# Kernel tuning notes

Measured on AMD Instinct MI355X. Metric: run time of the kernel, lower is better.

Reference implementation:

```python
import jax, jax.numpy as jnp
from jax import lax
import numpy as np

CONF_THRES = 0.55
IOU_THRES = 0.45
MAX_DET = 1000
MAX_WH = 7680.0   # class offset for class-aware NMS (agnostic=False)
K = 4096          # NMS candidate cap (yolov5 max_nms analogue, jit-static)
IMG = 640         # letterboxed network input size
B, N, NC = 16, 25200, 80


def setup_inputs() -> dict:
    key = jax.random.key(0)
    k1, k2, k3, k4 = jax.random.split(key, 4)
    cxcy = jax.random.uniform(k1, (B, N, 2), jnp.float32, 0.0, IMG)
    wh = jax.random.uniform(k2, (B, N, 2), jnp.float32, 2.0, 120.0)
    obj = jax.random.uniform(k3, (B, N, 1), jnp.float32) ** 4
    cls = jax.random.uniform(k4, (B, N, NC), jnp.float32)
    pred = jnp.concatenate([cxcy, wh, obj, cls], axis=-1)  # [B, N, 5+NC]
    return {"pred": pred, "img0_h": 1080, "img0_w": 1920}


def xywh2xyxy(x):
    cx, cy, w, h = x[..., 0], x[..., 1], x[..., 2], x[..., 3]
    return jnp.stack([cx - w / 2, cy - h / 2, cx + w / 2, cy + h / 2], axis=-1)


def box_iou(a, b):
    # a: [K,4], b: [K,4] xyxy -> [K,K]
    lt = jnp.maximum(a[:, None, :2], b[None, :, :2])
    rb = jnp.minimum(a[:, None, 2:], b[None, :, 2:])
    wh = jnp.clip(rb - lt, 0.0)
    inter = wh[..., 0] * wh[..., 1]
    area_a = (a[:, 2] - a[:, 0]) * (a[:, 3] - a[:, 1])
    area_b = (b[:, 2] - b[:, 0]) * (b[:, 3] - b[:, 1])
    return inter / (area_a[:, None] + area_b[None, :] - inter + 1e-7)


def _nms_image(p, img0_h, img0_w):
    # p: [N, 5+NC]
    obj = p[:, 4]
    cls_conf = p[:, 5:] * obj[:, None]          # conf = obj * cls
    conf = cls_conf.max(axis=-1)
    cls_id = cls_conf.argmax(axis=-1)
    valid = (obj > CONF_THRES) & (conf > CONF_THRES)
    score = jnp.where(valid, conf, -1.0)
    # top-K candidates, sorted by confidence (descending)
    top_scores, top_idx = lax.top_k(score, K)
    boxes = xywh2xyxy(p[top_idx, :4])           # [K,4]
    cl = cls_id[top_idx].astype(p.dtype)        # [K]
    iou = box_iou(boxes + cl[:, None] * MAX_WH, boxes + cl[:, None] * MAX_WH)
    idx = jnp.arange(K)
    keep0 = top_scores > 0.0

    def body(i, keep):
        # suppress i if a higher-scoring kept box overlaps it too much
        sup = jnp.any(keep & (idx < i) & (iou[:, i] > IOU_THRES))
        return keep.at[i].set(keep[i] & ~sup)

    keep = lax.fori_loop(0, K, body, keep0)
    kept_score = jnp.where(keep, top_scores, -1.0)
    fs, fi = lax.top_k(kept_score, MAX_DET)
    fb = boxes[fi]                              # [MAX_DET,4]
    fc = cl[fi]
    fvalid = fs > 0.0
    # scale_boxes: letterboxed 640x640 -> original img0
    gain = min(IMG / img0_h, IMG / img0_w)
    pad_x = (IMG - img0_w * gain) / 2
    pad_y = (IMG - img0_h * gain) / 2
    fb = (fb - jnp.array([pad_x, pad_y, pad_x, pad_y], fb.dtype)) / gain
    fb = jnp.clip(fb, 0.0, jnp.array([img0_w, img0_h, img0_w, img0_h], fb.dtype))
    fb = jnp.round(fb)
    det = jnp.concatenate([fb, fs[:, None], fc[:, None]], axis=-1)  # [MAX_DET,6]
    return jnp.where(fvalid[:, None], det, 0.0)


def reference(pred, img0_h, img0_w):
    return jax.vmap(lambda p: _nms_image(p, img0_h, img0_w))(pred)
```

## Files before the change

### kernel.cpp

```cpp
#include <hip/hip_runtime.h>

#define BB 16
#define NN 25200
#define NC 80
#define ROWL 85
#define KTOP 4096
#define MAXDET 1000
#define CONF_T 0.55f
#define IOU_T 0.45f
#define MAX_WH_F 7680.0f
#define CNT_STRIDE 32
#define PCNT_STRIDE 16
#define CCAP 256
#define NBIN 2048

#define OFF_CNT   81920
#define OFF_KCNT  83968
#define OFF_BUCK  86016
#define OFF_KEPT  2707456
#define ZERO_WORDS 21504

__global__ void zero_kernel(unsigned int* __restrict__ w) {
  w[blockIdx.x * 256 + threadIdx.x] = 0u;
}

__global__ __launch_bounds__(256) void score_kernel(const float* __restrict__ pred,
                             unsigned long long* __restrict__ buckets,
                             unsigned int* __restrict__ pcnt,
                             unsigned int* __restrict__ cnt) {
  const int b = blockIdx.y;
  const int lane = threadIdx.x & 63;
  const int a0 = blockIdx.x * 256 + (threadIdx.x & ~63);
  const int a = a0 + lane;
  const int g = lane >> 3;
  const int gl = lane & 7;
  const float* __restrict__ pb = pred + (size_t)b * NN * ROWL;
  float obj = 0.0f;
  if (a < NN) obj = pb[(size_t)a * ROWL + 4];
  unsigned long long mask = __ballot(obj > CONF_T);
  unsigned int nvacc = 0;
  while (mask) {
    unsigned long long sv = 0ull;
    #pragma unroll
    for (int q = 0; q < 8; ++q) {
      int sq = 255;
      if (mask) { sq = __ffsll(mask) - 1; mask &= mask - 1; }
      sv |= (unsigned long long)(unsigned)sq << (8 * q);
    }
    const int s0v = (int)(sv & 0xFF);
    const int sgv = (int)((sv >> (8 * g)) & 0xFF);
    const bool act = (sgv != 255);
    const int srow = act ? sgv : s0v;
    const int aa = a0 + srow;
    const float objg = __shfl(obj, srow, 64);
    const float* __restrict__ row = pb + (size_t)aa * ROWL;
    float best = -1.0f; int bi = gl;
    #pragma unroll
    for (int u = 0; u < 10; ++u) {
      float v = row[5 + gl + 8 * u] * objg;
      if (v > best) { best = v; bi = gl + 8 * u; }
    }
    #pragma unroll
    for (int off = 1; off <= 4; off <<= 1) {
      float ov = __shfl_xor(best, off, 64);
      int oi = __shfl_xor(bi, off, 64);
      if (ov > best || (ov == best && oi < bi)) { best = ov; bi = oi; }
    }
    bool emit = act && (gl == 0) && (best > CONF_T);
    if (emit) {
      unsigned long long key =
          ((unsigned long long)__float_as_uint(best) << 32) |
          ((unsigned long long)((~(unsigned)aa) & 0xFFFFu) << 16) |
          (unsigned long long)(unsigned)bi;
      unsigned int slot = atomicAdd(&pcnt[(b * NC + bi) * PCNT_STRIDE], 1u);
      if (slot < CCAP)
        buckets[((size_t)(b * NC + bi) << 8) + slot] = key;
    }
    unsigned long long em = __ballot(emit);
    if (lane == 0) nvacc += (unsigned int)__popcll(em);
  }
  if (lane == 0 && nvacc)
    atomicAdd(&cnt[b * CNT_STRIDE], nvacc);
}

__device__ __forceinline__ bool iou_sup(float ax1, float ay1, float ax2, float ay2,
                                        float aar, float bx1, float by1, float bx2,
                                        float by2, float bar) {
  float ltx = fmaxf(ax1, bx1), lty = fmaxf(ay1, by1);
  float rbx = fminf(ax2, bx2), rby = fminf(ay2, by2);
  float wv = rbx - ltx; wv = wv > 0.0f ? wv : 0.0f;
  float hv = rby - lty; hv = hv > 0.0f ? hv : 0.0f;
  float inter = wv * hv;
  float iou = inter / (aar + bar - inter + 1e-7f);
  return iou > IOU_T;
}

__global__ __launch_bounds__(64) void class_nms_kernel(
    const float* __restrict__ pred,
    const unsigned long long* __restrict__ buckets,
    const unsigned int* __restrict__ pcnt,
    const unsigned int* __restrict__ cnt,
    unsigned long long* __restrict__ kept,
    unsigned int* __restrict__ kcnt) {
  const int c = blockIdx.x;
  const int b = blockIdx.y;
  const int lane = threadIdx.x;
  const unsigned long long* __restrict__ bk = buckets + ((size_t)(b * NC + c) << 8);
  unsigned long long v0 = bk[lane];
  unsigned int pc = pcnt[(b * NC + c) * PCNT_STRIDE];
  const int count = (int)cnt[b * CNT_STRIDE];
  int n_c = (int)(pc < (unsigned)CCAP ? pc : (unsigned)CCAP);
  const float* __restrict__ pb = pred + (size_t)b * NN * ROWL;
  const float offc = (float)c * MAX_WH_F;

  if (n_c == 0) return;

  if (n_c <= 64 && count <= KTOP) {
    if (lane >= n_c) v0 = 0ull;
    for (int k2 = 2; k2 <= 64; k2 <<= 1) {
      for (int j = k2 >> 1; j >= 1; j >>= 1) {
        unsigned long long vo = __shfl_xor(v0, j, 64);
        bool desc = ((lane & k2) == 0);
        bool low = ((lane & j) == 0);
        if ((desc == low) ? (vo > v0) : (vo < v0)) v0 = vo;
      }
    }
    float x1 = 0.f, y1 = 0.f, x2 = 0.f, y2 = 0.f, aar = 0.f;
    const bool inr = (lane < n_c);
    if (inr) {
      unsigned int lo = (unsigned int)v0;
      int aa = (int)((~(lo >> 16)) & 0xFFFFu);
      const float* row = pb + (size_t)aa * ROWL;
      float cx = row[0], cy = row[1], w2 = row[2], h2 = row[3];
      x1 = (cx - w2 / 2.0f) + offc;
      y1 = (cy - h2 / 2.0f) + offc;
      x2 = (cx + w2 / 2.0f) + offc;
      y2 = (cy + h2 / 2.0f) + offc;
      aar = (x2 - x1) * (y2 - y1);
    }
    unsigned long long rowreg = 0ull;
    for (int i2 = 0; i2 < n_c; ++i2) {
      float bx1 = __shfl(x1, i2, 64), by1 = __shfl(y1, i2, 64);
      float bx2 = __shfl(x2, i2, 64), by2 = __shfl(y2, i2, 64);
      float bar = __shfl(aar, i2, 64);
      bool sup = inr && (lane > i2) &&
                 iou_sup(bx1, by1, bx2, by2, bar, x1, y1, x2, y2, aar);
      unsigned long long rm = __ballot(sup);
      if (lane == i2) rowreg = rm;
    }
    unsigned long long cand = (n_c >= 64) ? ~0ull : ((1ull << n_c) - 1ull);
    unsigned long long keepm = 0ull;
    while (cand) {
      int i = __ffsll(cand) - 1;
      keepm |= (1ull << i);
      unsigned long long rowi = __shfl(rowreg, i, 64);
      cand &= ~rowi;
      cand &= ~(1ull << i);
    }
    int keep0 = (int)((keepm >> lane) & 1ull);
    unsigned long long m0 = __ballot(keep0 != 0);
    int tot = (int)__popcll(m0);
    unsigned int base3 = 0;
    if (lane == 0) base3 = atomicAdd(&kcnt[b * CNT_STRIDE], (unsigned int)tot);
    base3 = (unsigned int)__shfl((int)base3, 0, 64);
    if (keep0) {
      unsigned int slot = base3 + (unsigned int)__popcll(m0 & ((1ull << lane) - 1ull));
      if (slot < (unsigned)KTOP) kept[(size_t)b * KTOP + slot] = v0;
    }
    return;
  }

  unsigned long long v[4];
  #pragma unroll
  for (int r = 0; r < 4; ++r) {
    int e = (r << 6) + lane;
    v[r] = (e < n_c) ? bk[e] : 0ull;
  }
  if (count > KTOP) {
    unsigned long long T = 0ull;
    for (int bit = 63; bit >= 0; --bit) {
      unsigned long long T2 = T | (1ull << bit);
      int cge = 0;
      for (int c2 = 0; c2 < NC; ++c2) {
        unsigned int p2 = pcnt[(b * NC + c2) * PCNT_STRIDE];
        int n2 = (int)(p2 < (unsigned)CCAP ? p2 : (unsigned)CCAP);
        const unsigned long long* bk2 = buckets + ((size_t)(b * NC + c2) << 8);
        for (int base2 = 0; base2 < n2; base2 += 64) {
          int i = base2 + lane;
          bool ge = (i < n2) && (bk2[i] >= T2);
          cge += (int)__popcll(__ballot(ge));
        }
      }
      if (cge >= KTOP) T = T2;
    }
    #pragma unroll
    for (int r = 0; r < 4; ++r) if (v[r] < T) v[r] = 0ull;
    n_c = 0;
    #pragma unroll
    for (int r = 0; r < 4; ++r) n_c += (int)__popcll(__ballot(v[r] != 0ull));
    if (n_c == 0) return;
  }
  for (int k2 = 2; k2 <= 256; k2 <<= 1) {
    if (k2 == 256) {
      #pragma unroll
      for (int r = 0; r < 2; ++r) {
        unsigned e = (unsigned)((r << 6) + lane);
        bool desc = ((e & k2) == 0);
        unsigned long long lo_ = v[r], hi_ = v[r + 2];
        bool sw = desc ? (lo_ < hi_) : (lo_ > hi_);
        v[r] = sw ? hi_ : lo_; v[r + 2] = sw ? lo_ : hi_;
      }
    }
    if (k2 >= 128) {
      #pragma unroll
      for (int rr = 0; rr < 2; ++rr) {
        int r = rr * 2;
        unsigned e = (unsigned)((r << 6) + lane);
        bool desc = ((e & k2) == 0);
        unsigned long long lo_ = v[r], hi_ = v[r + 1];
        bool sw = desc ? (lo_ < hi_) : (lo_ > hi_);
        v[r] = sw ? hi_ : lo_; v[r + 1] = sw ? lo_ : hi_;
      }
    }
    int j0 = (k2 >> 1) < 32 ? (k2 >> 1) : 32;
    for (int j = j0; j >= 1; j >>= 1) {
      #pragma unroll
      for (int r = 0; r < 4; ++r) {
        unsigned e = (unsigned)((r << 6) + lane);
        unsigned long long vo = __shfl_xor(v[r], j, 64);
        bool desc = ((e & k2) == 0);
        bool low = ((e & j) == 0);
        if ((desc == low) ? (vo > v[r]) : (vo < v[r])) v[r] = vo;
      }
    }
  }
  float x1r[4], y1r[4], x2r[4], y2r[4], ar[4];
  int keepr[4];
  #pragma unroll
  for (int r = 0; r < 4; ++r) {
    int e = (r << 6) + lane;
    keepr[r] = 0; x1r[r] = 0.f; y1r[r] = 0.f; x2r[r] = 0.f; y2r[r] = 0.f; ar[r] = 0.f;
    if (e < n_c) {
      unsigned int lo = (unsigned int)v[r];
      int aa = (int)((~(lo >> 16)) & 0xFFFFu);
      const float* row = pb + (size_t)aa * ROWL;
      float cx = row[0], cy = row[1], w2 = row[2], h2 = row[3];
      x1r[r] = (cx - w2 / 2.0f) + offc;
      y1r[r] = (cy - h2 / 2.0f) + offc;
      x2r[r] = (cx + w2 / 2.0f) + offc;
      y2r[r] = (cy + h2 / 2.0f) + offc;
      ar[r] = (x2r[r] - x1r[r]) * (y2r[r] - y1r[r]);
      keepr[r] = 1;
    }
  }
  for (int i2 = 0; i2 < n_c; ++i2) {
    int ci = i2 >> 6, li = i2 & 63;
    int ki; float bx1v, by1v, bx2v, by2v, bav;
    #define BCAST(R) { ki = __shfl(keepr[R], li, 64); bx1v = __shfl(x1r[R], li, 64); \
                       by1v = __shfl(y1r[R], li, 64); bx2v = __shfl(x2r[R], li, 64); \
                       by2v = __shfl(y2r[R], li, 64); bav = __shfl(ar[R], li, 64); }
    switch (ci) {
      case 0: BCAST(0); break;
      case 1: BCAST(1); break;
      case 2: BCAST(2); break;
      default: BCAST(3); break;
    }
    #undef BCAST
    if (!ki) continue;
    #pragma unroll
    for (int r = 0; r < 4; ++r) {
      int e = (r << 6) + lane;
      if (keepr[r] && e > i2 &&
          iou_sup(bx1v, by1v, bx2v, by2v, bav, x1r[r], y1r[r], x2r[r], y2r[r], ar[r]))
        keepr[r] = 0;
    }
  }
  unsigned long long m[4];
  int tot = 0;
  #pragma unroll
  for (int r = 0; r < 4; ++r) {
    m[r] = __ballot(keepr[r] != 0);
    tot += (int)__popcll(m[r]);
  }
  unsigned int base3 = 0;
  if (lane == 0) base3 = atomicAdd(&kcnt[b * CNT_STRIDE], (unsigned int)tot);
  base3 = (unsigned int)__shfl((int)base3, 0, 64);
  unsigned int start = base3;
  #pragma unroll
  for (int r = 0; r < 4; ++r) {
    if (keepr[r]) {
      unsigned int slot = start + (unsigned int)__popcll(m[r] & ((1ull << lane) - 1ull));
      if (slot < (unsigned)KTOP) kept[(size_t)b * KTOP + slot] = v[r];
    }
    start += (unsigned int)__popcll(m[r]);
  }
}

__global__ __launch_bounds__(1024) void finalize_kernel(
    const float* __restrict__ pred,
    const unsigned long long* __restrict__ kept,
    const unsigned int* __restrict__ kcnt,
    const int* __restrict__ ihp, const int* __restrict__ iwp,
    float* __restrict__ out) {
  __shared__ unsigned int hist[NBIN];
  __shared__ unsigned int sufx[NBIN];
  __shared__ unsigned int curs[NBIN];
  __shared__ unsigned int wsum[16], woff[16];
  __shared__ unsigned long long skey[KTOP];
  const int b = blockIdx.x;
  const int tid = threadIdx.x;
  const int lane = tid & 63;
  const int w = tid >> 6;
  unsigned int kcr = kcnt[b * CNT_STRIDE];
  const int kc = (int)(kcr < (unsigned)KTOP ? kcr : (unsigned)KTOP);
  const unsigned long long* __restrict__ kb = kept + (size_t)b * KTOP;

  hist[2 * tid] = 0u; hist[2 * tid + 1] = 0u;
  __syncthreads();

  unsigned long long myk[4];
  int myb[4];
  #pragma unroll
  for (int r = 0; r < 4; ++r) {
    int i = tid + (r << 10);
    myb[r] = -1; myk[r] = 0ull;
    if (i < kc) {
      unsigned long long k = kb[i];
      int bin = (int)((k >> 44) & (unsigned long long)(NBIN - 1));
      myk[r] = k; myb[r] = bin;
      atomicAdd(&hist[bin], 1u);
    }
  }
  __syncthreads();

  unsigned int h0 = hist[2 * tid], h1 = hist[2 * tid + 1];
  unsigned int v = h0 + h1;
  #pragma unroll
  for (int off = 1; off < 64; off <<= 1) {
    unsigned int o = __shfl_down(v, off, 64);
    if (lane + off < 64) v += o;
  }
  if (lane == 0) wsum[w] = v;
  __syncthreads();
  if (tid < 16) {
    unsigned int s = 0;
    for (int j = tid + 1; j < 16; ++j) s += wsum[j];
    woff[tid] = s;
  }
  __syncthreads();
  unsigned int incl = v + woff[w];
  unsigned int excl = incl - (h0 + h1);
  sufx[2 * tid] = excl + h1;
  sufx[2 * tid + 1] = excl;
  curs[2 * tid] = excl + h1;
  curs[2 * tid + 1] = excl;
  __syncthreads();

  #pragma unroll
  for (int r = 0; r < 4; ++r) {
    if (myb[r] >= 0) {
      unsigned int p = atomicAdd(&curs[myb[r]], 1u);
      skey[p] = myk[r];
    }
  }
  __syncthreads();

  const int h = ihp[0], w3 = iwp[0];
  const double gd = fmin(640.0 / (double)h, 640.0 / (double)w3);
  const float gain = (float)gd;
  const float padx = (float)((640.0 - (double)w3 * gd) * 0.5);
  const float pady = (float)((640.0 - (double)h * gd) * 0.5);
  const float wf = (float)w3, hf = (float)h;
  #pragma unroll
  for (int r = 0; r < 4; ++r) {
    if (myb[r] >= 0) {
      unsigned long long k = myk[r];
      unsigned int gstart = sufx[myb[r]];
      unsigned int gcnt = hist[myb[r]];
      unsigned int rank = gstart;
      for (unsigned int j = 0; j < gcnt; ++j)
        rank += (skey[gstart + j] > k) ? 1u : 0u;
      if (rank < MAXDET) {
        unsigned int lo = (unsigned int)k;
        int aa = (int)((~(lo >> 16)) & 0xFFFFu);
        int cls = (int)(lo & 0xFFFFu);
        float score = __uint_as_float((unsigned int)(k >> 32));
        const float* row = pred + ((size_t)b * NN + aa) * ROWL;
        float cx = row[0], cy = row[1], wd = row[2], ht = row[3];
        float x1 = cx - wd / 2.0f, y1 = cy - ht / 2.0f;
        float x2 = cx + wd / 2.0f, y2 = cy + ht / 2.0f;
        x1 = rintf(fminf(fmaxf((x1 - padx) / gain, 0.0f), wf));
        y1 = rintf(fminf(fmaxf((y1 - pady) / gain, 0.0f), hf));
        x2 = rintf(fminf(fmaxf((x2 - padx) / gain, 0.0f), wf));
        y2 = rintf(fminf(fmaxf((y2 - pady) / gain, 0.0f), hf));
        float* o = out + ((size_t)b * MAXDET + (int)rank) * 6;
        o[0] = x1; o[1] = y1; o[2] = x2; o[3] = y2;
        o[4] = score; o[5] = (float)cls;
      }
    }
  }
  for (int i = kc + tid; i < MAXDET; i += 1024) {
    float* o = out + ((size_t)b * MAXDET + i) * 6;
    o[0] = 0.0f; o[1] = 0.0f; o[2] = 0.0f; o[3] = 0.0f; o[4] = 0.0f; o[5] = 0.0f;
  }
}

extern "C" void kernel_launch(void* const* d_in, const int* in_sizes, int n_in,
                              void* d_out, int out_size, void* d_ws, size_t ws_size,
                              hipStream_t stream) {
  const float* pred = (const float*)d_in[0];
  const int* ih = (const int*)d_in[1];
  const int* iw = (const int*)d_in[2];
  float* out = (float*)d_out;
  char* ws = (char*)d_ws;

  unsigned int* pcnt = (unsigned int*)ws;
  unsigned int* cnt = (unsigned int*)(ws + OFF_CNT);
  unsigned int* kcnt = (unsigned int*)(ws + OFF_KCNT);
  unsigned long long* buckets = (unsigned long long*)(ws + OFF_BUCK);
  unsigned long long* kept = (unsigned long long*)(ws + OFF_KEPT);

  zero_kernel<<<ZERO_WORDS / 256, 256, 0, stream>>>((unsigned int*)ws);
  dim3 sgrid((NN + 255) / 256, BB);
  score_kernel<<<sgrid, 256, 0, stream>>>(pred, buckets, pcnt, cnt);
  dim3 cgrid(NC, BB);
  class_nms_kernel<<<cgrid, 64, 0, stream>>>(pred, buckets, pcnt, cnt, kept, kcnt);
  finalize_kernel<<<BB, 1024, 0, stream>>>(pred, kept, kcnt, ih, iw, out);
}
```

Measured before the change: 74.68 us.

## Fuse class bucketing, per-class NMS and finalize into one per-image kernel

The scoring kernel now writes a dense key per anchor without atomics. A single 1024-thread block per image compacts valid keys into LDS, buckets them by class, runs per-class NMS across its 16 waves and then does the final ranking and output. This removes the zero-fill kernel, the global atomics and the global bucket/kept buffers, and cuts the launch count from four to two. In exchange the per-class NMS work is spread over only 16 blocks instead of 1280, and a full-size key array must be round-tripped through global memory.

```diff
diff --git a/kernel.cpp b/kernel.cpp
--- a/kernel.cpp
+++ b/kernel.cpp
@@ -9,78 +9,38 @@
 #define CONF_T 0.55f
 #define IOU_T 0.45f
 #define MAX_WH_F 7680.0f
-#define CNT_STRIDE 32
-#define PCNT_STRIDE 16
-#define CCAP 256
+#define CAPV 8192
+#define CCAP 128
 #define NBIN 2048
 
-#define OFF_CNT   81920
-#define OFF_KCNT  83968
-#define OFF_BUCK  86016
-#define OFF_KEPT  2707456
-#define ZERO_WORDS 21504
-
-__global__ void zero_kernel(unsigned int* __restrict__ w) {
-  w[blockIdx.x * 256 + threadIdx.x] = 0u;
-}
-
 __global__ __launch_bounds__(256) void score_kernel(const float* __restrict__ pred,
-                             unsigned long long* __restrict__ buckets,
-                             unsigned int* __restrict__ pcnt,
-                             unsigned int* __restrict__ cnt) {
+                                                    unsigned long long* __restrict__ gkey) {
   const int b = blockIdx.y;
-  const int lane = threadIdx.x & 63;
-  const int a0 = blockIdx.x * 256 + (threadIdx.x & ~63);
-  const int a = a0 + lane;
-  const int g = lane >> 3;
-  const int gl = lane & 7;
-  const float* __restrict__ pb = pred + (size_t)b * NN * ROWL;
-  float obj = 0.0f;
-  if (a < NN) obj = pb[(size_t)a * ROWL + 4];
-  unsigned long long mask = __ballot(obj > CONF_T);
-  unsigned int nvacc = 0;
-  while (mask) {
-    unsigned long long sv = 0ull;
+  const int a = blockIdx.x * 256 + threadIdx.x;
+  if (a >= NN) return;
+  const float* __restrict__ row = pred + ((size_t)b * NN + a) * ROWL;
+  unsigned long long key = 0ull;
+  float obj = row[4];
+  if (obj > CONF_T) {
+    float b0 = -1.0f, b1 = -1.0f, b2 = -1.0f, b3 = -1.0f;
+    int i0 = 0, i1 = 20, i2 = 40, i3 = 60;
     #pragma unroll
-    for (int q = 0; q < 8; ++q) {
-      int sq = 255;
-      if (mask) { sq = __ffsll(mask) - 1; mask &= mask - 1; }
-      sv |= (unsigned long long)(unsigned)sq << (8 * q);
-    }
-    const int s0v = (int)(sv & 0xFF);
-    const int sgv = (int)((sv >> (8 * g)) & 0xFF);
-    const bool act = (sgv != 255);
-    const int srow = act ? sgv : s0v;
-    const int aa = a0 + srow;
-    const float objg = __shfl(obj, srow, 64);
-    const float* __restrict__ row = pb + (size_t)aa * ROWL;
-    float best = -1.0f; int bi = gl;
-    #pragma unroll
-    for (int u = 0; u < 10; ++u) {
-      float v = row[5 + gl + 8 * u] * objg;
-      if (v > best) { best = v; bi = gl + 8 * u; }
-    }
-    #pragma unroll
-    for (int off = 1; off <= 4; off <<= 1) {
-      float ov = __shfl_xor(best, off, 64);
-      int oi = __shfl_xor(bi, off, 64);
-      if (ov > best || (ov == best && oi < bi)) { best = ov; bi = oi; }
-    }
-    bool emit = act && (gl == 0) && (best > CONF_T);
-    if (emit) {
-      unsigned long long key =
-          ((unsigned long long)__float_as_uint(best) << 32) |
-          ((unsigned long long)((~(unsigned)aa) & 0xFFFFu) << 16) |
-          (unsigned long long)(unsigned)bi;
-      unsigned int slot = atomicAdd(&pcnt[(b * NC + bi) * PCNT_STRIDE], 1u);
-      if (slot < CCAP)
-        buckets[((size_t)(b * NC + bi) << 8) + slot] = key;
-    }
-    unsigned long long em = __ballot(emit);
-    if (lane == 0) nvacc += (unsigned int)__popcll(em);
-  }
-  if (lane == 0 && nvacc)
-    atomicAdd(&cnt[b * CNT_STRIDE], nvacc);
+    for (int t = 0; t < 20; ++t) {
+      float v0 = row[5 + t] * obj;  if (v0 > b0) { b0 = v0; i0 = t; }
+      float v1 = row[25 + t] * obj; if (v1 > b1) { b1 = v1; i1 = 20 + t; }
+      float v2 = row[45 + t] * obj; if (v2 > b2) { b2 = v2; i2 = 40 + t; }
+      float v3 = row[65 + t] * obj; if (v3 > b3) { b3 = v3; i3 = 60 + t; }
+    }
+    float best = b0; int bi = i0;
+    if (b1 > best) { best = b1; bi = i1; }
+    if (b2 > best) { best = b2; bi = i2; }
+    if (b3 > best) { best = b3; bi = i3; }
+    if (best > CONF_T)
+      key = ((unsigned long long)__float_as_uint(best) << 32) |
+            ((unsigned long long)((~(unsigned)a) & 0xFFFFu) << 16) |
+            (unsigned long long)(unsigned)bi;
+  }
+  gkey[(size_t)b * NN + a] = key;
 }
 
 __device__ __forceinline__ bool iou_sup(float ax1, float ay1, float ax2, float ay2,
@@ -95,225 +55,249 @@
   return iou > IOU_T;
 }
 
-__global__ __launch_bounds__(64) void class_nms_kernel(
+__global__ __launch_bounds__(1024) void image_kernel(
     const float* __restrict__ pred,
-    const unsigned long long* __restrict__ buckets,
-    const unsigned int* __restrict__ pcnt,
-    const unsigned int* __restrict__ cnt,
-    unsigned long long* __restrict__ kept,
-    unsigned int* __restrict__ kcnt) {
-  const int c = blockIdx.x;
-  const int b = blockIdx.y;
-  const int lane = threadIdx.x;
-  const unsigned long long* __restrict__ bk = buckets + ((size_t)(b * NC + c) << 8);
-  unsigned long long v0 = bk[lane];
-  unsigned int pc = pcnt[(b * NC + c) * PCNT_STRIDE];
-  const int count = (int)cnt[b * CNT_STRIDE];
-  int n_c = (int)(pc < (unsigned)CCAP ? pc : (unsigned)CCAP);
-  const float* __restrict__ pb = pred + (size_t)b * NN * ROWL;
-  const float offc = (float)c * MAX_WH_F;
-
-  if (n_c == 0) return;
-
-  if (n_c <= 64 && count <= KTOP) {
-    if (lane >= n_c) v0 = 0ull;
-    for (int k2 = 2; k2 <= 64; k2 <<= 1) {
-      for (int j = k2 >> 1; j >= 1; j >>= 1) {
-        unsigned long long vo = __shfl_xor(v0, j, 64);
-        bool desc = ((lane & k2) == 0);
-        bool low = ((lane & j) == 0);
-        if ((desc == low) ? (vo > v0) : (vo < v0)) v0 = vo;
-      }
-    }
-    float x1 = 0.f, y1 = 0.f, x2 = 0.f, y2 = 0.f, aar = 0.f;
-    const bool inr = (lane < n_c);
-    if (inr) {
-      unsigned int lo = (unsigned int)v0;
-      int aa = (int)((~(lo >> 16)) & 0xFFFFu);
-      const float* row = pb + (size_t)aa * ROWL;
-      float cx = row[0], cy = row[1], w2 = row[2], h2 = row[3];
-      x1 = (cx - w2 / 2.0f) + offc;
-      y1 = (cy - h2 / 2.0f) + offc;
-      x2 = (cx + w2 / 2.0f) + offc;
-      y2 = (cy + h2 / 2.0f) + offc;
-      aar = (x2 - x1) * (y2 - y1);
-    }
-    unsigned long long rowreg = 0ull;
-    for (int i2 = 0; i2 < n_c; ++i2) {
-      float bx1 = __shfl(x1, i2, 64), by1 = __shfl(y1, i2, 64);
-      float bx2 = __shfl(x2, i2, 64), by2 = __shfl(y2, i2, 64);
-      float bar = __shfl(aar, i2, 64);
-      bool sup = inr && (lane > i2) &&
-                 iou_sup(bx1, by1, bx2, by2, bar, x1, y1, x2, y2, aar);
-      unsigned long long rm = __ballot(sup);
-      if (lane == i2) rowreg = rm;
-    }
-    unsigned long long cand = (n_c >= 64) ? ~0ull : ((1ull << n_c) - 1ull);
-    unsigned long long keepm = 0ull;
-    while (cand) {
-      int i = __ffsll(cand) - 1;
-      keepm |= (1ull << i);
-      unsigned long long rowi = __shfl(rowreg, i, 64);
-      cand &= ~rowi;
-      cand &= ~(1ull << i);
-    }
-    int keep0 = (int)((keepm >> lane) & 1ull);
-    unsigned long long m0 = __ballot(keep0 != 0);
-    int tot = (int)__popcll(m0);
-    unsigned int base3 = 0;
-    if (lane == 0) base3 = atomicAdd(&kcnt[b * CNT_STRIDE], (unsigned int)tot);
-    base3 = (unsigned int)__shfl((int)base3, 0, 64);
-    if (keep0) {
-      unsigned int slot = base3 + (unsigned int)__popcll(m0 & ((1ull << lane) - 1ull));
-      if (slot < (unsigned)KTOP) kept[(size_t)b * KTOP + slot] = v0;
-    }
-    return;
-  }
-
-  unsigned long long v[4];
-  #pragma unroll
-  for (int r = 0; r < 4; ++r) {
-    int e = (r << 6) + lane;
-    v[r] = (e < n_c) ? bk[e] : 0ull;
-  }
-  if (count > KTOP) {
-    unsigned long long T = 0ull;
-    for (int bit = 63; bit >= 0; --bit) {
-      unsigned long long T2 = T | (1ull << bit);
-      int cge = 0;
-      for (int c2 = 0; c2 < NC; ++c2) {
-        unsigned int p2 = pcnt[(b * NC + c2) * PCNT_STRIDE];
-        int n2 = (int)(p2 < (unsigned)CCAP ? p2 : (unsigned)CCAP);
-        const unsigned long long* bk2 = buckets + ((size_t)(b * NC + c2) << 8);
-        for (int base2 = 0; base2 < n2; base2 += 64) {
-          int i = base2 + lane;
-          bool ge = (i < n2) && (bk2[i] >= T2);
-          cge += (int)__popcll(__ballot(ge));
-        }
-      }
-      if (cge >= KTOP) T = T2;
-    }
-    #pragma unroll
-    for (int r = 0; r < 4; ++r) if (v[r] < T) v[r] = 0ull;
-    n_c = 0;
-    #pragma unroll
-    for (int r = 0; r < 4; ++r) n_c += (int)__popcll(__ballot(v[r] != 0ull));
-    if (n_c == 0) return;
-  }
-  for (int k2 = 2; k2 <= 256; k2 <<= 1) {
-    if (k2 == 256) {
-      #pragma unroll
-      for (int r = 0; r < 2; ++r) {
-        unsigned e = (unsigned)((r << 6) + lane);
-        bool desc = ((e & k2) == 0);
-        unsigned long long lo_ = v[r], hi_ = v[r + 2];
-        bool sw = desc ? (lo_ < hi_) : (lo_ > hi_);
-        v[r] = sw ? hi_ : lo_; v[r + 2] = sw ? lo_ : hi_;
-      }
-    }
-    if (k2 >= 128) {
-      #pragma unroll
-      for (int rr = 0; rr < 2; ++rr) {
-        int r = rr * 2;
-        unsigned e = (unsigned)((r << 6) + lane);
-        bool desc = ((e & k2) == 0);
-        unsigned long long lo_ = v[r], hi_ = v[r + 1];
-        bool sw = desc ? (lo_ < hi_) : (lo_ > hi_);
-        v[r] = sw ? hi_ : lo_; v[r + 1] = sw ? lo_ : hi_;
-      }
-    }
-    int j0 = (k2 >> 1) < 32 ? (k2 >> 1) : 32;
-    for (int j = j0; j >= 1; j >>= 1) {
-      #pragma unroll
-      for (int r = 0; r < 4; ++r) {
-        unsigned e = (unsigned)((r << 6) + lane);
-        unsigned long long vo = __shfl_xor(v[r], j, 64);
-        bool desc = ((e & k2) == 0);
-        bool low = ((e & j) == 0);
-        if ((desc == low) ? (vo > v[r]) : (vo < v[r])) v[r] = vo;
-      }
-    }
-  }
-  float x1r[4], y1r[4], x2r[4], y2r[4], ar[4];
-  int keepr[4];
-  #pragma unroll
-  for (int r = 0; r < 4; ++r) {
-    int e = (r << 6) + lane;
-    keepr[r] = 0; x1r[r] = 0.f; y1r[r] = 0.f; x2r[r] = 0.f; y2r[r] = 0.f; ar[r] = 0.f;
-    if (e < n_c) {
-      unsigned int lo = (unsigned int)v[r];
-      int aa = (int)((~(lo >> 16)) & 0xFFFFu);
-      const float* row = pb + (size_t)aa * ROWL;
-      float cx = row[0], cy = row[1], w2 = row[2], h2 = row[3];
-      x1r[r] = (cx - w2 / 2.0f) + offc;
-      y1r[r] = (cy - h2 / 2.0f) + offc;
-      x2r[r] = (cx + w2 / 2.0f) + offc;
-      y2r[r] = (cy + h2 / 2.0f) + offc;
-      ar[r] = (x2r[r] - x1r[r]) * (y2r[r] - y1r[r]);
-      keepr[r] = 1;
-    }
-  }
-  for (int i2 = 0; i2 < n_c; ++i2) {
-    int ci = i2 >> 6, li = i2 & 63;
-    int ki; float bx1v, by1v, bx2v, by2v, bav;
-    #define BCAST(R) { ki = __shfl(keepr[R], li, 64); bx1v = __shfl(x1r[R], li, 64); \
-                       by1v = __shfl(y1r[R], li, 64); bx2v = __shfl(x2r[R], li, 64); \
-                       by2v = __shfl(y2r[R], li, 64); bav = __shfl(ar[R], li, 64); }
-    switch (ci) {
-      case 0: BCAST(0); break;
-      case 1: BCAST(1); break;
-      case 2: BCAST(2); break;
-      default: BCAST(3); break;
-    }
-    #undef BCAST
-    if (!ki) continue;
-    #pragma unroll
-    for (int r = 0; r < 4; ++r) {
-      int e = (r << 6) + lane;
-      if (keepr[r] && e > i2 &&
-          iou_sup(bx1v, by1v, bx2v, by2v, bav, x1r[r], y1r[r], x2r[r], y2r[r], ar[r]))
-        keepr[r] = 0;
-    }
-  }
-  unsigned long long m[4];
-  int tot = 0;
-  #pragma unroll
-  for (int r = 0; r < 4; ++r) {
-    m[r] = __ballot(keepr[r] != 0);
-    tot += (int)__popcll(m[r]);
-  }
-  unsigned int base3 = 0;
-  if (lane == 0) base3 = atomicAdd(&kcnt[b * CNT_STRIDE], (unsigned int)tot);
-  base3 = (unsigned int)__shfl((int)base3, 0, 64);
-  unsigned int start = base3;
-  #pragma unroll
-  for (int r = 0; r < 4; ++r) {
-    if (keepr[r]) {
-      unsigned int slot = start + (unsigned int)__popcll(m[r] & ((1ull << lane) - 1ull));
-      if (slot < (unsigned)KTOP) kept[(size_t)b * KTOP + slot] = v[r];
-    }
-    start += (unsigned int)__popcll(m[r]);
-  }
-}
-
-__global__ __launch_bounds__(1024) void finalize_kernel(
-    const float* __restrict__ pred,
-    const unsigned long long* __restrict__ kept,
-    const unsigned int* __restrict__ kcnt,
+    const unsigned long long* __restrict__ gkey,
     const int* __restrict__ ihp, const int* __restrict__ iwp,
     float* __restrict__ out) {
-  __shared__ unsigned int hist[NBIN];
-  __shared__ unsigned int sufx[NBIN];
-  __shared__ unsigned int curs[NBIN];
+  __shared__ unsigned long long vkeys[CAPV];
+  __shared__ unsigned long long cbuck[NC * CCAP];
+  __shared__ unsigned int ccnt[NC];
+  __shared__ unsigned int redbuf[16];
   __shared__ unsigned int wsum[16], woff[16];
-  __shared__ unsigned long long skey[KTOP];
+  __shared__ unsigned int vcnt, kcnt;
   const int b = blockIdx.x;
   const int tid = threadIdx.x;
   const int lane = tid & 63;
   const int w = tid >> 6;
-  unsigned int kcr = kcnt[b * CNT_STRIDE];
-  const int kc = (int)(kcr < (unsigned)KTOP ? kcr : (unsigned)KTOP);
-  const unsigned long long* __restrict__ kb = kept + (size_t)b * KTOP;
+  const float* __restrict__ pb = pred + (size_t)b * NN * ROWL;
+  const unsigned long long* __restrict__ gk = gkey + (size_t)b * NN;
+
+  if (tid == 0) { vcnt = 0u; kcnt = 0u; }
+  if (tid < NC) ccnt[tid] = 0u;
+  __syncthreads();
+
+  for (int seg = w; seg < (NN + 63) / 64; seg += 16) {
+    int i = seg * 64 + lane;
+    unsigned long long k = (i < NN) ? gk[i] : 0ull;
+    bool pr = (k != 0ull);
+    unsigned long long m = __ballot(pr);
+    int nv = (int)__popcll(m);
+    unsigned int base = 0;
+    if (nv) {
+      if (lane == 0) base = atomicAdd(&vcnt, (unsigned int)nv);
+      base = (unsigned int)__shfl((int)base, 0, 64);
+      if (pr) {
+        unsigned int slot = base + (unsigned int)__popcll(m & ((1ull << lane) - 1ull));
+        if (slot < (unsigned)CAPV) vkeys[slot] = k;
+      }
+    }
+  }
+  __syncthreads();
+
+  const unsigned int count = vcnt;
+  const int nv2 = (int)(count < (unsigned)CAPV ? count : (unsigned)CAPV);
+
+  if (count > (unsigned)KTOP) {
+    unsigned long long T = 0ull;
+    for (int bit = 63; bit >= 0; --bit) {
+      unsigned long long T2 = T | (1ull << bit);
+      unsigned int c = 0;
+      for (int i = tid; i < nv2; i += 1024) c += (vkeys[i] >= T2) ? 1u : 0u;
+      #pragma unroll
+      for (int off = 32; off >= 1; off >>= 1) c += __shfl_down(c, off, 64);
+      if (lane == 0) redbuf[w] = c;
+      __syncthreads();
+      unsigned int total = 0;
+      for (int j = 0; j < 16; ++j) total += redbuf[j];
+      if (total >= (unsigned)KTOP) T = T2;
+      __syncthreads();
+    }
+    for (int i = tid; i < nv2; i += 1024) if (vkeys[i] < T) vkeys[i] = 0ull;
+    __syncthreads();
+  }
+
+  for (int i = tid; i < nv2; i += 1024) {
+    unsigned long long k = vkeys[i];
+    if (k) {
+      int cls = (int)(k & 0xFFFFu);
+      unsigned int slot = atomicAdd(&ccnt[cls], 1u);
+      if (slot < (unsigned)CCAP) cbuck[cls * CCAP + slot] = k;
+    }
+  }
+  __syncthreads();
+
+  #pragma unroll 1
+  for (int cc = 0; cc < 5; ++cc) {
+    const int c = w + (cc << 4);
+    unsigned int pcv = ccnt[c];
+    int n_c = (int)(pcv < (unsigned)CCAP ? pcv : (unsigned)CCAP);
+    if (n_c == 0) continue;
+    const unsigned long long* __restrict__ bkc = &cbuck[c * CCAP];
+    const float offc = (float)c * MAX_WH_F;
+
+    if (n_c <= 64) {
+      unsigned long long v0 = (lane < n_c) ? bkc[lane] : 0ull;
+      for (int k2 = 2; k2 <= 64; k2 <<= 1) {
+        for (int j = k2 >> 1; j >= 1; j >>= 1) {
+          unsigned long long vo = __shfl_xor(v0, j, 64);
+          bool desc = ((lane & k2) == 0);
+          bool low = ((lane & j) == 0);
+          if ((desc == low) ? (vo > v0) : (vo < v0)) v0 = vo;
+        }
+      }
+      float x1 = 0.f, y1 = 0.f, x2 = 0.f, y2 = 0.f, aar = 0.f;
+      const bool inr = (lane < n_c);
+      if (inr) {
+        unsigned int lo = (unsigned int)v0;
+        int aa = (int)((~(lo >> 16)) & 0xFFFFu);
+        const float* row = pb + (size_t)aa * ROWL;
+        float cx = row[0], cy = row[1], w2 = row[2], h2 = row[3];
+        x1 = (cx - w2 / 2.0f) + offc;
+        y1 = (cy - h2 / 2.0f) + offc;
+        x2 = (cx + w2 / 2.0f) + offc;
+        y2 = (cy + h2 / 2.0f) + offc;
+        aar = (x2 - x1) * (y2 - y1);
+      }
+      unsigned long long rowreg = 0ull;
+      for (int i2 = 0; i2 < n_c; ++i2) {
+        float bx1 = __shfl(x1, i2, 64), by1 = __shfl(y1, i2, 64);
+        float bx2 = __shfl(x2, i2, 64), by2 = __shfl(y2, i2, 64);
+        float bar = __shfl(aar, i2, 64);
+        bool sup = inr && (lane > i2) &&
+                   iou_sup(bx1, by1, bx2, by2, bar, x1, y1, x2, y2, aar);
+        unsigned long long rm = __ballot(sup);
+        if (lane == i2) rowreg = rm;
+      }
+      unsigned long long cand = (n_c >= 64) ? ~0ull : ((1ull << n_c) - 1ull);
+      unsigned long long keepm = 0ull;
+      while (cand) {
+        int i = __ffsll(cand) - 1;
+        keepm |= (1ull << i);
+        unsigned long long rowi = __shfl(rowreg, i, 64);
+        cand &= ~rowi;
+        cand &= ~(1ull << i);
+      }
+      int keep0 = (int)((keepm >> lane) & 1ull);
+      unsigned long long m0 = __ballot(keep0 != 0);
+      int tot = (int)__popcll(m0);
+      unsigned int base3 = 0;
+      if (lane == 0) base3 = atomicAdd(&kcnt, (unsigned int)tot);
+      base3 = (unsigned int)__shfl((int)base3, 0, 64);
+      if (keep0) {
+        unsigned int slot = base3 + (unsigned int)__popcll(m0 & ((1ull << lane) - 1ull));
+        if (slot < (unsigned)KTOP) vkeys[slot] = v0;
+      }
+    } else {
+      unsigned long long v[4];
+      #pragma unroll
+      for (int r = 0; r < 4; ++r) {
+        int e = (r << 6) + lane;
+        v[r] = (e < n_c) ? bkc[e] : 0ull;
+      }
+      for (int k2 = 2; k2 <= 256; k2 <<= 1) {
+        if (k2 == 256) {
+          #pragma unroll
+          for (int r = 0; r < 2; ++r) {
+            unsigned e = (unsigned)((r << 6) + lane);
+            bool desc = ((e & k2) == 0);
+            unsigned long long lo_ = v[r], hi_ = v[r + 2];
+            bool sw = desc ? (lo_ < hi_) : (lo_ > hi_);
+            v[r] = sw ? hi_ : lo_; v[r + 2] = sw ? lo_ : hi_;
+          }
+        }
+        if (k2 >= 128) {
+          #pragma unroll
+          for (int rr = 0; rr < 2; ++rr) {
+            int r = rr * 2;
+            unsigned e = (unsigned)((r << 6) + lane);
+            bool desc = ((e & k2) == 0);
+            unsigned long long lo_ = v[r], hi_ = v[r + 1];
+            bool sw = desc ? (lo_ < hi_) : (lo_ > hi_);
+            v[r] = sw ? hi_ : lo_; v[r + 1] = sw ? lo_ : hi_;
+          }
+        }
+        int j0 = (k2 >> 1) < 32 ? (k2 >> 1) : 32;
+        for (int j = j0; j >= 1; j >>= 1) {
+          #pragma unroll
+          for (int r = 0; r < 4; ++r) {
+            unsigned e = (unsigned)((r << 6) + lane);
+            unsigned long long vo = __shfl_xor(v[r], j, 64);
+            bool desc = ((e & k2) == 0);
+            bool low = ((e & j) == 0);
+            if ((desc == low) ? (vo > v[r]) : (vo < v[r])) v[r] = vo;
+          }
+        }
+      }
+      float x1r[4], y1r[4], x2r[4], y2r[4], ar[4];
+      int keepr[4];
+      #pragma unroll
+      for (int r = 0; r < 4; ++r) {
+        int e = (r << 6) + lane;
+        keepr[r] = 0; x1r[r] = 0.f; y1r[r] = 0.f; x2r[r] = 0.f; y2r[r] = 0.f; ar[r] = 0.f;
+        if (e < n_c) {
+          unsigned int lo = (unsigned int)v[r];
+          int aa = (int)((~(lo >> 16)) & 0xFFFFu);
+          const float* row = pb + (size_t)aa * ROWL;
+          float cx = row[0], cy = row[1], w2 = row[2], h2 = row[3];
+          x1r[r] = (cx - w2 / 2.0f) + offc;
+          y1r[r] = (cy - h2 / 2.0f) + offc;
+          x2r[r] = (cx + w2 / 2.0f) + offc;
+          y2r[r] = (cy + h2 / 2.0f) + offc;
+          ar[r] = (x2r[r] - x1r[r]) * (y2r[r] - y1r[r]);
+          keepr[r] = 1;
+        }
+      }
+      for (int i2 = 0; i2 < n_c; ++i2) {
+        int ci = i2 >> 6, li = i2 & 63;
+        int ki; float bx1v, by1v, bx2v, by2v, bav;
+        #define BCAST(R) { ki = __shfl(keepr[R], li, 64); bx1v = __shfl(x1r[R], li, 64); \
+                           by1v = __shfl(y1r[R], li, 64); bx2v = __shfl(x2r[R], li, 64); \
+                           by2v = __shfl(y2r[R], li, 64); bav = __shfl(ar[R], li, 64); }
+        switch (ci) {
+          case 0: BCAST(0); break;
+          case 1: BCAST(1); break;
+          case 2: BCAST(2); break;
+          default: BCAST(3); break;
+        }
+        #undef BCAST
+        if (!ki) continue;
+        #pragma unroll
+        for (int r = 0; r < 4; ++r) {
+          int e = (r << 6) + lane;
+          if (keepr[r] && e > i2 &&
+              iou_sup(bx1v, by1v, bx2v, by2v, bav, x1r[r], y1r[r], x2r[r], y2r[r], ar[r]))
+            keepr[r] = 0;
+        }
+      }
+      unsigned long long m[4];
+      int tot = 0;
+      #pragma unroll
+      for (int r = 0; r < 4; ++r) {
+        m[r] = __ballot(keepr[r] != 0);
+        tot += (int)__popcll(m[r]);
+      }
+      unsigned int base3 = 0;
+      if (lane == 0) base3 = atomicAdd(&kcnt, (unsigned int)tot);
+      base3 = (unsigned int)__shfl((int)base3, 0, 64);
+      unsigned int start = base3;
+      #pragma unroll
+      for (int r = 0; r < 4; ++r) {
+        if (keepr[r]) {
+          unsigned int slot = start + (unsigned int)__popcll(m[r] & ((1ull << lane) - 1ull));
+          if (slot < (unsigned)KTOP) vkeys[slot] = v[r];
+        }
+        start += (unsigned int)__popcll(m[r]);
+      }
+    }
+  }
+  __syncthreads();
+
+  unsigned int* hist = (unsigned int*)cbuck;
+  unsigned int* sufx = hist + NBIN;
+  unsigned int* curs = hist + 2 * NBIN;
+  unsigned long long* skey = (unsigned long long*)(hist + 3 * NBIN);
+  const int kc = (int)(kcnt < (unsigned)KTOP ? kcnt : (unsigned)KTOP);
 
   hist[2 * tid] = 0u; hist[2 * tid + 1] = 0u;
   __syncthreads();
@@ -325,7 +309,7 @@
     int i = tid + (r << 10);
     myb[r] = -1; myk[r] = 0ull;
     if (i < kc) {
-      unsigned long long k = kb[i];
+      unsigned long long k = vkeys[i];
       int bin = (int)((k >> 44) & (unsigned long long)(NBIN - 1));
       myk[r] = k; myb[r] = bin;
       atomicAdd(&hist[bin], 1u);
@@ -385,7 +369,7 @@
         int aa = (int)((~(lo >> 16)) & 0xFFFFu);
         int cls = (int)(lo & 0xFFFFu);
         float score = __uint_as_float((unsigned int)(k >> 32));
-        const float* row = pred + ((size_t)b * NN + aa) * ROWL;
+        const float* row = pb + (size_t)aa * ROWL;
         float cx = row[0], cy = row[1], wd = row[2], ht = row[3];
         float x1 = cx - wd / 2.0f, y1 = cy - ht / 2.0f;
         float x2 = cx + wd / 2.0f, y2 = cy + ht / 2.0f;
@@ -412,18 +396,9 @@
   const int* ih = (const int*)d_in[1];
   const int* iw = (const int*)d_in[2];
   float* out = (float*)d_out;
-  char* ws = (char*)d_ws;
-
-  unsigned int* pcnt = (unsigned int*)ws;
-  unsigned int* cnt = (unsigned int*)(ws + OFF_CNT);
-  unsigned int* kcnt = (unsigned int*)(ws + OFF_KCNT);
-  unsigned long long* buckets = (unsigned long long*)(ws + OFF_BUCK);
-  unsigned long long* kept = (unsigned long long*)(ws + OFF_KEPT);
-
-  zero_kernel<<<ZERO_WORDS / 256, 256, 0, stream>>>((unsigned int*)ws);
+  unsigned long long* gkey = (unsigned long long*)d_ws;
+
   dim3 sgrid((NN + 255) / 256, BB);
-  score_kernel<<<sgrid, 256, 0, stream>>>(pred, buckets, pcnt, cnt);
-  dim3 cgrid(NC, BB);
-  class_nms_kernel<<<cgrid, 64, 0, stream>>>(pred, buckets, pcnt, cnt, kept, kcnt);
-  finalize_kernel<<<BB, 1024, 0, stream>>>(pred, kept, kcnt, ih, iw, out);
+  score_kernel<<<sgrid, 256, 0, stream>>>(pred, gkey);
+  image_kernel<<<BB, 1024, 0, stream>>>(pred, gkey, ih, iw, out);
 }
```

Result: slower. 165.4 us (+121.5%).
